# Kernel tuning notes

Hardware: AMD Instinct MI355X
Metric: run time of the kernel (lower is better)

Reference implementation:

```python
import jax, jax.numpy as jnp
import numpy as np

DIM = 512
HIDDEN = 2048
D_M = 256
R = 64
GEN_HIDDEN = D_M * 2  # hidden_mul=2
ALPHA_MEM = 1.0


def setup_inputs() -> dict:
    key = jax.random.key(0)
    ks = jax.random.split(key, 12)
    B, T = 2, 512
    inp = {
        'x': jax.random.normal(ks[0], (B, T, DIM), jnp.float32),
        'm_tok': jax.random.normal(ks[1], (B, T, D_M), jnp.float32),
        # base SwiGLU params
        'W1': jax.random.normal(ks[2], (HIDDEN, DIM), jnp.float32) * (1.0 / np.sqrt(DIM)),
        'W2': jax.random.normal(ks[3], (HIDDEN, DIM), jnp.float32) * (1.0 / np.sqrt(DIM)),
        'W3': jax.random.normal(ks[4], (DIM, HIDDEN), jnp.float32) * (1.0 / np.sqrt(HIDDEN)),
        'b1': jnp.zeros((HIDDEN,), jnp.float32),
        'b2': jnp.zeros((HIDDEN,), jnp.float32),
        'b3': jnp.zeros((DIM,), jnp.float32),
        # hypernetwork (FFNMemGenerator): d_m -> gen_hidden -> 3*r*dim
        'gen_w1': jax.random.normal(ks[5], (GEN_HIDDEN, D_M), jnp.float32) * (1.0 / np.sqrt(D_M)),
        'gen_b1': jnp.zeros((GEN_HIDDEN,), jnp.float32),
        'gen_w2': jax.random.normal(ks[6], (3 * R * DIM, GEN_HIDDEN), jnp.float32) * (0.02 / np.sqrt(GEN_HIDDEN)),
        'gen_b2': jnp.zeros((3 * R * DIM,), jnp.float32),
        'mem_gate': jnp.zeros((), jnp.float32),
    }
    return inp


def reference(x, m_tok, W1, W2, W3, b1, b2, b3, gen_w1, gen_b1, gen_w2, gen_b2, mem_gate):
    B, T, _ = x.shape
    # base SwiGLU FFN
    x1 = jnp.einsum('od,btd->bto', W1, x) + b1  # [B,T,hidden]
    x2 = jnp.einsum('od,btd->bto', W2, x) + b2
    h_base = jax.nn.silu(x1) * x2
    y_base = jnp.einsum('do,bto->btd', W3, h_base) + b3  # [B,T,dim]

    # hypernetwork-generated per-token low-rank weights
    hg = jax.nn.silu(jnp.einsum('hd,btd->bth', gen_w1, m_tok) + gen_b1)
    w = jnp.einsum('oh,bth->bto', gen_w2, hg) + gen_b2  # [B,T,3*r*dim]
    W1_m = w[..., : R * DIM].reshape(B, T, R, DIM)
    W2_m = w[..., R * DIM : 2 * R * DIM].reshape(B, T, R, DIM)
    W3_m = w[..., 2 * R * DIM :].reshape(B, T, DIM, R)

    # per-token batched matvecs (memory path)
    u1 = jnp.einsum('btrd,btd->btr', W1_m, x)
    u2 = jnp.einsum('btrd,btd->btr', W2_m, x)
    h_mem = jax.nn.silu(u1) * u2
    y_mem = jnp.einsum('btdr,btr->btd', W3_m, h_mem)

    g = jax.nn.sigmoid(mem_gate)
    return y_base + g * ALPHA_MEM * y_mem
```

## Files before the change

### kernel.cpp

```cpp
#include <hip/hip_runtime.h>
#include <cstdint>
#include <cstddef>

#define TOK   1024
#define DIMX  512
#define HID   2048
#define DM    256
#define GENH  512
#define RR    64
#define O3BASE 65536

typedef __bf16 bf16x8 __attribute__((ext_vector_type(8)));
typedef float  f32x4  __attribute__((ext_vector_type(4)));

__device__ __forceinline__ unsigned short f2bf(float f) {
  union { float f; uint32_t u; } v; v.f = f;
  return (unsigned short)((v.u + 0x7fffu + ((v.u >> 16) & 1u)) >> 16);
}
__device__ __forceinline__ float bf2f(unsigned short h) {
  union { uint32_t u; float f; } v; v.u = (uint32_t)h << 16;
  return v.f;
}
__device__ __forceinline__ float silu_f(float x) { return x / (1.f + __expf(-x)); }

__device__ __forceinline__ void async_copy16(const void* g, void* l) {
  __builtin_amdgcn_global_load_lds(
      (const __attribute__((address_space(1))) void*)g,
      (__attribute__((address_space(3))) void*)l, 16, 0, 0);
}

__device__ __forceinline__ void cast8(const float* __restrict__ src,
                                      unsigned short* __restrict__ dst, size_t i) {
  float4 v0 = *(const float4*)(src + i);
  float4 v1 = *(const float4*)(src + i + 4);
  ushort4 h0, h1;
  h0.x = f2bf(v0.x); h0.y = f2bf(v0.y); h0.z = f2bf(v0.z); h0.w = f2bf(v0.w);
  h1.x = f2bf(v1.x); h1.y = f2bf(v1.y); h1.z = f2bf(v1.z); h1.w = f2bf(v1.w);
  *(ushort4*)(dst + i)     = h0;
  *(ushort4*)(dst + i + 4) = h1;
}

__global__ __launch_bounds__(256) void cast_bf16_kernel(
    const float* __restrict__ src, unsigned short* __restrict__ dst) {
  cast8(src, dst, ((size_t)blockIdx.x * 256 + threadIdx.x) * 8);
}

template<int ROWS>
__device__ __forceinline__ void stage_tile(
    const unsigned short* __restrict__ base, size_t row0, int stride, int kofs,
    unsigned short* Ls, int tid) {
  constexpr int IT = ROWS / 32;
  const int wave = tid >> 6, lane = tid & 63;
#pragma unroll
  for (int j = 0; j < IT; ++j) {
    int s   = wave * (IT * 64) + j * 64 + lane;
    int row = s >> 3;
    int kc  = (s & 7) ^ (row & 7);
    const unsigned short* g = base + (row0 + (size_t)row) * (size_t)stride + kofs + kc * 8;
    async_copy16(g, (char*)Ls + wave * (IT * 1024) + j * 1024);
  }
}

template<int KLEN, int MF>
__device__ __forceinline__ void mfma_tile_nt(
    const unsigned short* __restrict__ Abf, size_t a_row0, int astride,
    const unsigned short* __restrict__ Bbf, size_t b_row0, int bstride, int k0,
    unsigned short* As, unsigned short* Bs, f32x4 (&acc)[MF][4]) {
  const int tid  = threadIdx.x;
  const int lane = tid & 63;
  const int wave = tid >> 6;
  const int m0 = (wave >> 1) * (MF * 16), n0 = (wave & 1) * 64;

  for (int kk = 0; kk < KLEN; kk += 64) {
    stage_tile<MF * 32>(Abf, a_row0, astride, k0 + kk, As, tid);
    stage_tile<128>(Bbf, b_row0, bstride, k0 + kk, Bs, tid);
    __syncthreads();
#pragma unroll
    for (int ks = 0; ks < 2; ++ks) {
      int cbase = ks * 4 + (lane >> 4);
      int koff  = (cbase ^ (lane & 7)) * 8;
      bf16x8 a[MF], b[4];
#pragma unroll
      for (int mf = 0; mf < MF; ++mf)
        a[mf] = *(const bf16x8*)(As + (m0 + mf * 16 + (lane & 15)) * 64 + koff);
#pragma unroll
      for (int nf = 0; nf < 4; ++nf)
        b[nf] = *(const bf16x8*)(Bs + (n0 + nf * 16 + (lane & 15)) * 64 + koff);
#pragma unroll
      for (int mf = 0; mf < MF; ++mf)
#pragma unroll
        for (int nf = 0; nf < 4; ++nf)
          acc[mf][nf] = __builtin_amdgcn_mfma_f32_16x16x32_bf16(
              a[mf], b[nf], acc[mf][nf], 0, 0, 0);
    }
    __syncthreads();
  }
}

template<int MF>
__device__ __forceinline__ void zero_accN(f32x4 (&acc)[MF][4]) {
#pragma unroll
  for (int i = 0; i < MF; ++i)
#pragma unroll
    for (int j = 0; j < 4; ++j) {
      f32x4 z = {0.f, 0.f, 0.f, 0.f};
      acc[i][j] = z;
    }
}

__global__ __launch_bounds__(256) void prep_kernel(
    const float* __restrict__ x, const float* __restrict__ m_tok,
    const float* __restrict__ gen_w1, const float* __restrict__ gen_b1,
    const float* __restrict__ W1, const float* __restrict__ W2,
    const float* __restrict__ W3,
    unsigned short* __restrict__ xb, unsigned short* __restrict__ hgb,
    unsigned short* __restrict__ W1b, unsigned short* __restrict__ W2b,
    unsigned short* __restrict__ W3b) {
  __shared__ float mt[4 * DM];
  const int tid = threadIdx.x;
  const size_t t0 = (size_t)blockIdx.x * 4;
#pragma unroll
  for (int k = 0; k < 4; ++k) mt[k * 256 + tid] = m_tok[t0 * DM + k * 256 + tid];
#pragma unroll
  for (int k = 0; k < 8; ++k) {
    size_t idx = t0 * DIMX + k * 256 + tid;
    xb[idx] = f2bf(x[idx]);
  }
  {
    size_t base = ((size_t)blockIdx.x * 256 + tid) * 8;
#pragma unroll
    for (int it = 0; it < 2; ++it) {
      size_t idx = base + (size_t)it * 524288;
      cast8(W1, W1b, idx);
      cast8(W2, W2b, idx);
      cast8(W3, W3b, idx);
    }
  }
  __syncthreads();
#pragma unroll
  for (int hh = 0; hh < 2; ++hh) {
    int h = hh * 256 + tid;
    float a0, a1, a2, a3;
    a0 = a1 = a2 = a3 = gen_b1[h];
    const float* wr = gen_w1 + (size_t)h * DM;
    for (int d = 0; d < DM; d += 4) {
      float4 w = *(const float4*)(wr + d);
      a0 += w.x * mt[d]       + w.y * mt[d + 1]       + w.z * mt[d + 2]       + w.w * mt[d + 3];
      a1 += w.x * mt[256 + d] + w.y * mt[256 + d + 1] + w.z * mt[256 + d + 2] + w.w * mt[256 + d + 3];
      a2 += w.x * mt[512 + d] + w.y * mt[512 + d + 1] + w.z * mt[512 + d + 2] + w.w * mt[512 + d + 3];
      a3 += w.x * mt[768 + d] + w.y * mt[768 + d + 1] + w.z * mt[768 + d + 2] + w.w * mt[768 + d + 3];
    }
    hgb[(t0 + 0) * GENH + h] = f2bf(silu_f(a0));
    hgb[(t0 + 1) * GENH + h] = f2bf(silu_f(a1));
    hgb[(t0 + 2) * GENH + h] = f2bf(silu_f(a2));
    hgb[(t0 + 3) * GENH + h] = f2bf(silu_f(a3));
  }
}

__global__ __launch_bounds__(256) void ffn12_kernel(
    const unsigned short* __restrict__ xb, const unsigned short* __restrict__ W1b,
    const unsigned short* __restrict__ W2b, const float* __restrict__ pb1,
    const float* __restrict__ pb2, unsigned short* __restrict__ hb) {
  __shared__ unsigned short As[32 * 64];
  __shared__ unsigned short B1s[128 * 64];
  __shared__ unsigned short B2s[128 * 64];
  const int tid = threadIdx.x, lane = tid & 63, wave = tid >> 6;
  const int ob = blockIdx.x & 15, tb = blockIdx.x >> 4;
  const size_t t0 = (size_t)tb * 32, o0 = (size_t)ob * 128;
  const int m0 = (wave >> 1) * 16, n0 = (wave & 1) * 64;

  f32x4 acc1[4], acc2[4];
#pragma unroll
  for (int j = 0; j < 4; ++j) {
    f32x4 z = {0.f, 0.f, 0.f, 0.f};
    acc1[j] = z; acc2[j] = z;
  }

  for (int kk = 0; kk < DIMX; kk += 64) {
    stage_tile<32>(xb, t0, DIMX, kk, As, tid);
    stage_tile<128>(W1b, o0, DIMX, kk, B1s, tid);
    stage_tile<128>(W2b, o0, DIMX, kk, B2s, tid);
    __syncthreads();
#pragma unroll
    for (int ks = 0; ks < 2; ++ks) {
      int cbase = ks * 4 + (lane >> 4);
      int koff  = (cbase ^ (lane & 7)) * 8;
      bf16x8 a, b1[4], b2[4];
      a = *(const bf16x8*)(As + (m0 + (lane & 15)) * 64 + koff);
#pragma unroll
      for (int nf = 0; nf < 4; ++nf) {
        b1[nf] = *(const bf16x8*)(B1s + (n0 + nf * 16 + (lane & 15)) * 64 + koff);
        b2[nf] = *(const bf16x8*)(B2s + (n0 + nf * 16 + (lane & 15)) * 64 + koff);
      }
#pragma unroll
      for (int nf = 0; nf < 4; ++nf) {
        acc1[nf] = __builtin_amdgcn_mfma_f32_16x16x32_bf16(a, b1[nf], acc1[nf], 0, 0, 0);
        acc2[nf] = __builtin_amdgcn_mfma_f32_16x16x32_bf16(a, b2[nf], acc2[nf], 0, 0, 0);
      }
    }
    __syncthreads();
  }

  const int q = lane >> 4;
  float b1v[4], b2v[4];
#pragma unroll
  for (int nf = 0; nf < 4; ++nf) {
    b1v[nf] = pb1[o0 + n0 + nf * 16 + (lane & 15)];
    b2v[nf] = pb2[o0 + n0 + nf * 16 + (lane & 15)];
  }
#pragma unroll
  for (int nf = 0; nf < 4; ++nf)
#pragma unroll
    for (int rg = 0; rg < 4; ++rg) {
      size_t trow = t0 + m0 + q * 4 + rg;
      size_t col  = o0 + n0 + nf * 16 + (lane & 15);
      float v1 = acc1[nf][rg] + b1v[nf];
      float v2 = acc2[nf][rg] + b2v[nf];
      hb[trow * HID + col] = f2bf(silu_f(v1) * v2);
    }
}

__global__ __launch_bounds__(256) void gemm3p_kernel(
    const unsigned short* __restrict__ hb, const unsigned short* __restrict__ W3b,
    float* __restrict__ yp) {
  __shared__ unsigned short As[64 * 64];
  __shared__ unsigned short Bs[128 * 64];
  const int ob = blockIdx.x & 3, tb = blockIdx.x >> 2;
  const size_t o0 = (size_t)ob * 128, t0 = (size_t)tb * 64;
  const int k0 = blockIdx.y * 512;
  f32x4 acc[2][4];
  zero_accN<2>(acc);
  mfma_tile_nt<512, 2>(hb, t0, HID, W3b, o0, HID, k0, As, Bs, acc);

  const int tid = threadIdx.x, lane = tid & 63, wave = tid >> 6;
  const int m0 = (wave >> 1) * 32, n0 = (wave & 1) * 64;
  float* out = yp + (size_t)blockIdx.y * (TOK * DIMX);
#pragma unroll
  for (int nf = 0; nf < 4; ++nf) {
    int n = n0 + nf * 16 + (lane & 15);
#pragma unroll
    for (int mf = 0; mf < 2; ++mf) {
      int mb = m0 + mf * 16 + ((lane >> 4) << 2);
#pragma unroll
      for (int rg = 0; rg < 4; ++rg)
        out[(t0 + mb + rg) * DIMX + o0 + n] = acc[mf][nf][rg];
    }
  }
}

__global__ __launch_bounds__(256) void yreduce_kernel(
    const float* __restrict__ yp, const float* __restrict__ b3,
    float* __restrict__ ybase) {
  size_t i = ((size_t)blockIdx.x * 256 + threadIdx.x) * 4;
  int d = (int)(i & (DIMX - 1));
  float4 s = *(const float4*)(b3 + d);
#pragma unroll
  for (int p = 0; p < 4; ++p) {
    float4 v = *(const float4*)(yp + (size_t)p * (TOK * DIMX) + i);
    s.x += v.x; s.y += v.y; s.z += v.z; s.w += v.w;
  }
  *(float4*)(ybase + i) = s;
}

union SmemUV {
  struct { unsigned short As[8192], Bs[8192]; } ab;
  struct { unsigned short Xs[128 * 128]; } ep;
};

__global__ __launch_bounds__(256) void memuv_kernel(
    const unsigned short* __restrict__ hgb, const unsigned short* __restrict__ w2b,
    const float* __restrict__ gen_b2, const unsigned short* __restrict__ xb,
    float* __restrict__ up) {
  __shared__ SmemUV sm;
  const int bx = blockIdx.x;
  const int s8 = bx & 7, w = bx >> 3;
  const int tb = w & 7, strip = (w >> 3) * 8 + s8;
  const size_t o0 = (size_t)strip * 128, t0 = (size_t)tb * 128;
  const int j  = strip >> 2;
  const int d0 = (strip & 3) * 128;

  f32x4 acc[4][4];
  zero_accN<4>(acc);
  mfma_tile_nt<GENH, 4>(hgb, t0, GENH, w2b, o0, GENH, 0, sm.ab.As, sm.ab.Bs, acc);

  const int tid = threadIdx.x, lane = tid & 63, wave = tid >> 6;
#pragma unroll
  for (int i = 0; i < 8; ++i) {
    int qq = i * 256 + tid;
    int row = qq >> 4, c = qq & 15;
    const unsigned short* src = xb + (t0 + (size_t)row) * DIMX + d0 + c * 8;
    ushort4 v0 = *(const ushort4*)src;
    ushort4 v1 = *(const ushort4*)(src + 4);
    int cs = c ^ (((row >> 2) & 3) << 1);
    unsigned short* dst = sm.ep.Xs + row * 128 + cs * 8;
    *(ushort4*)dst = v0;
    *(ushort4*)(dst + 4) = v1;
  }
  __syncthreads();

  const int m0 = (wave >> 1) * 64, n0 = (wave & 1) * 64;
  const int q = lane >> 4, l15 = lane & 15;
  float gbv[4];
#pragma unroll
  for (int i = 0; i < 4; ++i)
    gbv[i] = gen_b2[o0 + n0 + i * 16 + l15];

  const int p = (strip & 3) * 2 + (wave & 1);
  float* upd = up + (size_t)p * (128 * 1024) + (size_t)j * 1024 + t0;
#pragma unroll
  for (int mf = 0; mf < 4; ++mf) {
    f32x4 vals;
#pragma unroll
    for (int rg = 0; rg < 4; ++rg) {
      int trow = m0 + mf * 16 + q * 4 + rg;
      int swz  = ((trow >> 2) & 3) << 1;
      float val = 0.f;
#pragma unroll
      for (int nf = 0; nf < 4; ++nf) {
        int col = n0 + nf * 16 + l15;
        int idx = trow * 128 + (((col >> 3) ^ swz) << 3) + (col & 7);
        val += (acc[mf][nf][rg] + gbv[nf]) * bf2f(sm.ep.Xs[idx]);
      }
      val += __shfl_xor(val, 1);
      val += __shfl_xor(val, 2);
      val += __shfl_xor(val, 4);
      val += __shfl_xor(val, 8);
      vals[rg] = val;
    }
    if (l15 == 0)
      *(f32x4*)(upd + m0 + mf * 16 + q * 4) = vals;
  }
}

__global__ __launch_bounds__(256) void hmem_kernel(
    const float* __restrict__ up, float* __restrict__ hm) {
  int i = blockIdx.x * 256 + threadIdx.x;
  int t = i & 1023, r = i >> 10;
  float u1 = 0.f, u2 = 0.f;
#pragma unroll
  for (int p = 0; p < 8; ++p) {
    u1 += up[(size_t)p * (128 * 1024) + (size_t)r * 1024 + t];
    u2 += up[(size_t)p * (128 * 1024) + (size_t)(64 + r) * 1024 + t];
  }
  hm[(size_t)t * RR + r] = silu_f(u1) * u2;
}

union SmemY {
  struct { unsigned short As[8192], Bs[8192]; } ab;
  struct { float Hs[128 * 64]; } ep;
};

__global__ __launch_bounds__(256) void memy_kernel(
    const unsigned short* __restrict__ hgb, const unsigned short* __restrict__ w2b,
    const float* __restrict__ gen_b2, const float* __restrict__ hmem,
    const float* __restrict__ ybase, const float* __restrict__ mem_gate,
    float* __restrict__ y) {
  __shared__ SmemY sm;
  const int bx = blockIdx.x;
  const int s8 = bx & 7, w = bx >> 3;
  const int tb = w & 7, strip = (w >> 3) * 8 + s8;
  const size_t brow0 = (size_t)O3BASE + (size_t)strip * 128;
  const size_t t0 = (size_t)tb * 128;

  f32x4 acc[4][4];
  zero_accN<4>(acc);
  mfma_tile_nt<GENH, 4>(hgb, t0, GENH, w2b, brow0, GENH, 0, sm.ab.As, sm.ab.Bs, acc);

  const int tid = threadIdx.x, lane = tid & 63, wave = tid >> 6;
#pragma unroll
  for (int i = 0; i < 8; ++i) {
    int qq = i * 256 + tid;
    int row = qq >> 4, c = qq & 15;
    float4 v = *(const float4*)(hmem + (t0 + (size_t)row) * RR + c * 4);
    int cs = c ^ (((row >> 2) & 3) << 2);
    *(float4*)(sm.ep.Hs + row * 64 + cs * 4) = v;
  }
  __syncthreads();

  const int m0 = (wave >> 1) * 64, n0 = (wave & 1) * 64;
  const int q = lane >> 4, l15 = lane & 15;
  const float g = 1.f / (1.f + __expf(-mem_gate[0]));
  float gbv[4];
#pragma unroll
  for (int i = 0; i < 4; ++i)
    gbv[i] = gen_b2[brow0 + n0 + i * 16 + l15];

  const int d = strip * 2 + (wave & 1);
#pragma unroll
  for (int mf = 0; mf < 4; ++mf)
#pragma unroll
    for (int rg = 0; rg < 4; ++rg) {
      int trow = m0 + mf * 16 + q * 4 + rg;
      int swz  = ((trow >> 2) & 3) << 2;
      float val = 0.f;
#pragma unroll
      for (int nf = 0; nf < 4; ++nf) {
        int r = nf * 16 + l15;
        int idx = trow * 64 + (((r >> 2) ^ swz) << 2) + (r & 3);
        val += (acc[mf][nf][rg] + gbv[nf]) * sm.ep.Hs[idx];
      }
      val += __shfl_xor(val, 1);
      val += __shfl_xor(val, 2);
      val += __shfl_xor(val, 4);
      val += __shfl_xor(val, 8);
      if (l15 == 0) {
        size_t gi = (t0 + trow) * DIMX + d;
        y[gi] = ybase[gi] + g * val;
      }
    }
}

extern "C" void kernel_launch(void* const* d_in, const int* in_sizes, int n_in,
                              void* d_out, int out_size, void* d_ws, size_t ws_size,
                              hipStream_t stream) {
  const float* x        = (const float*)d_in[0];
  const float* m_tok    = (const float*)d_in[1];
  const float* W1       = (const float*)d_in[2];
  const float* W2       = (const float*)d_in[3];
  const float* W3       = (const float*)d_in[4];
  const float* b1       = (const float*)d_in[5];
  const float* b2       = (const float*)d_in[6];
  const float* b3       = (const float*)d_in[7];
  const float* gen_w1   = (const float*)d_in[8];
  const float* gen_b1   = (const float*)d_in[9];
  const float* gen_w2   = (const float*)d_in[10];
  const float* gen_b2   = (const float*)d_in[11];
  const float* mem_gate = (const float*)d_in[12];
  float* y = (float*)d_out;

  char* ws = (char*)d_ws;
#define KB(v) ((size_t)(v) << 10)
  unsigned short* xb    = (unsigned short*)(ws);
  unsigned short* hgb   = (unsigned short*)(ws + KB(1024));
  unsigned short* hb    = (unsigned short*)(ws + KB(2048));
  float* up    = (float*)(ws + KB(6144));
  float* hm    = (float*)(ws + KB(10240));
  float* yp    = (float*)(ws + KB(10752));
  float* ybase = (float*)(ws + KB(19200));
  unsigned short* W1b = (unsigned short*)(ws + KB(21248));
  unsigned short* W2b = (unsigned short*)(ws + KB(23296));
  unsigned short* W3b = (unsigned short*)(ws + KB(25344));
  unsigned short* w2b = (unsigned short*)(ws + KB(27392));
#undef KB

  prep_kernel<<<256, 256, 0, stream>>>(x, m_tok, gen_w1, gen_b1, W1, W2, W3,
                                       xb, hgb, W1b, W2b, W3b);
  cast_bf16_kernel<<<24576, 256, 0, stream>>>(gen_w2, w2b);

  ffn12_kernel<<<512, 256, 0, stream>>>(xb, W1b, W2b, b1, b2, hb);
  gemm3p_kernel<<<dim3(64, 4), 256, 0, stream>>>(hb, W3b, yp);
  yreduce_kernel<<<512, 256, 0, stream>>>(yp, b3, ybase);

  memuv_kernel<<<4096, 256, 0, stream>>>(hgb, w2b, gen_b2, xb, up);
  hmem_kernel<<<256, 256, 0, stream>>>(up, hm);
  memy_kernel<<<2048, 256, 0, stream>>>(hgb, w2b, gen_b2, hm, ybase, mem_gate, y);
}
```

Before: 528.0 us.

## Fuse gen_w2 cast into GEMM staging and merge independent kernels

Removes the separate pass that casts gen_w2 from fp32 to bf16 and instead loads fp32 gen_w2 tiles inside the memuv/memy GEMMs, converting them to bf16 in registers before writing to LDS. The ffn12 and memuv kernels are merged into one launch, as are gemm3p and hmem, with branching on block index. The yreduce kernel is folded into memy's epilogue. This saves a large 24 MB write/read round trip and several launches, but the gen_w2 tile loads become synchronous and twice as wide, since gen_w2 is read in fp32 instead of bf16 with no async copy to LDS.

New measurement: 539.7 us. 2.2% more time.

```diff
diff --git a/kernel.cpp b/kernel.cpp
--- a/kernel.cpp
+++ b/kernel.cpp
@@ -22,6 +22,13 @@
   return v.f;
 }
 __device__ __forceinline__ float silu_f(float x) { return x / (1.f + __expf(-x)); }
+
+__device__ __forceinline__ ushort4 cvt4_hw(float4 v) {
+  union { __bf16 b; unsigned short u; } r0, r1, r2, r3;
+  r0.b = (__bf16)v.x; r1.b = (__bf16)v.y; r2.b = (__bf16)v.z; r3.b = (__bf16)v.w;
+  ushort4 h; h.x = r0.u; h.y = r1.u; h.z = r2.u; h.w = r3.u;
+  return h;
+}
 
 __device__ __forceinline__ void async_copy16(const void* g, void* l) {
   __builtin_amdgcn_global_load_lds(
@@ -40,11 +47,6 @@
   *(ushort4*)(dst + i + 4) = h1;
 }
 
-__global__ __launch_bounds__(256) void cast_bf16_kernel(
-    const float* __restrict__ src, unsigned short* __restrict__ dst) {
-  cast8(src, dst, ((size_t)blockIdx.x * 256 + threadIdx.x) * 8);
-}
-
 template<int ROWS>
 __device__ __forceinline__ void stage_tile(
     const unsigned short* __restrict__ base, size_t row0, int stride, int kofs,
@@ -74,6 +76,61 @@
   for (int kk = 0; kk < KLEN; kk += 64) {
     stage_tile<MF * 32>(Abf, a_row0, astride, k0 + kk, As, tid);
     stage_tile<128>(Bbf, b_row0, bstride, k0 + kk, Bs, tid);
+    __syncthreads();
+#pragma unroll
+    for (int ks = 0; ks < 2; ++ks) {
+      int cbase = ks * 4 + (lane >> 4);
+      int koff  = (cbase ^ (lane & 7)) * 8;
+      bf16x8 a[MF], b[4];
+#pragma unroll
+      for (int mf = 0; mf < MF; ++mf)
+        a[mf] = *(const bf16x8*)(As + (m0 + mf * 16 + (lane & 15)) * 64 + koff);
+#pragma unroll
+      for (int nf = 0; nf < 4; ++nf)
+        b[nf] = *(const bf16x8*)(Bs + (n0 + nf * 16 + (lane & 15)) * 64 + koff);
+#pragma unroll
+      for (int mf = 0; mf < MF; ++mf)
+#pragma unroll
+        for (int nf = 0; nf < 4; ++nf)
+          acc[mf][nf] = __builtin_amdgcn_mfma_f32_16x16x32_bf16(
+              a[mf], b[nf], acc[mf][nf], 0, 0, 0);
+    }
+    __syncthreads();
+  }
+}
+
+template<int KLEN, int MF>
+__device__ __forceinline__ void mfma_tile_nt_bf32(
+    const unsigned short* __restrict__ Abf, size_t a_row0, int astride,
+    const float* __restrict__ Bf, size_t b_row0, int bstride, int k0,
+    unsigned short* As, unsigned short* Bs, f32x4 (&acc)[MF][4]) {
+  const int tid  = threadIdx.x;
+  const int lane = tid & 63;
+  const int wave = tid >> 6;
+  const int m0 = (wave >> 1) * (MF * 16), n0 = (wave & 1) * 64;
+
+  for (int kk = 0; kk < KLEN; kk += 64) {
+    stage_tile<MF * 32>(Abf, a_row0, astride, k0 + kk, As, tid);
+#pragma unroll
+    for (int grp = 0; grp < 2; ++grp) {
+      float4 v[4];
+#pragma unroll
+      for (int jj = 0; jj < 2; ++jj) {
+        int s   = wave * 256 + (grp * 2 + jj) * 64 + lane;
+        int row = s >> 3;
+        int kc  = (s & 7) ^ (row & 7);
+        const float* g = Bf + (b_row0 + (size_t)row) * (size_t)bstride
+                            + (k0 + kk) + kc * 8;
+        v[2 * jj]     = *(const float4*)g;
+        v[2 * jj + 1] = *(const float4*)(g + 4);
+      }
+#pragma unroll
+      for (int jj = 0; jj < 2; ++jj) {
+        int s = wave * 256 + (grp * 2 + jj) * 64 + lane;
+        *(ushort4*)(Bs + s * 8)     = cvt4_hw(v[2 * jj]);
+        *(ushort4*)(Bs + s * 8 + 4) = cvt4_hw(v[2 * jj + 1]);
+      }
+    }
     __syncthreads();
 #pragma unroll
     for (int ks = 0; ks < 2; ++ks) {
@@ -157,15 +214,13 @@
   }
 }
 
-__global__ __launch_bounds__(256) void ffn12_kernel(
-    const unsigned short* __restrict__ xb, const unsigned short* __restrict__ W1b,
+__device__ __forceinline__ void ffn12_body(
+    int bx, const unsigned short* __restrict__ xb, const unsigned short* __restrict__ W1b,
     const unsigned short* __restrict__ W2b, const float* __restrict__ pb1,
-    const float* __restrict__ pb2, unsigned short* __restrict__ hb) {
-  __shared__ unsigned short As[32 * 64];
-  __shared__ unsigned short B1s[128 * 64];
-  __shared__ unsigned short B2s[128 * 64];
+    const float* __restrict__ pb2, unsigned short* __restrict__ hb,
+    unsigned short* As, unsigned short* B1s, unsigned short* B2s) {
   const int tid = threadIdx.x, lane = tid & 63, wave = tid >> 6;
-  const int ob = blockIdx.x & 15, tb = blockIdx.x >> 4;
+  const int ob = bx & 15, tb = bx >> 4;
   const size_t t0 = (size_t)tb * 32, o0 = (size_t)ob * 128;
   const int m0 = (wave >> 1) * 16, n0 = (wave & 1) * 64;
 
@@ -220,59 +275,15 @@
     }
 }
 
-__global__ __launch_bounds__(256) void gemm3p_kernel(
-    const unsigned short* __restrict__ hb, const unsigned short* __restrict__ W3b,
-    float* __restrict__ yp) {
-  __shared__ unsigned short As[64 * 64];
-  __shared__ unsigned short Bs[128 * 64];
-  const int ob = blockIdx.x & 3, tb = blockIdx.x >> 2;
-  const size_t o0 = (size_t)ob * 128, t0 = (size_t)tb * 64;
-  const int k0 = blockIdx.y * 512;
-  f32x4 acc[2][4];
-  zero_accN<2>(acc);
-  mfma_tile_nt<512, 2>(hb, t0, HID, W3b, o0, HID, k0, As, Bs, acc);
-
-  const int tid = threadIdx.x, lane = tid & 63, wave = tid >> 6;
-  const int m0 = (wave >> 1) * 32, n0 = (wave & 1) * 64;
-  float* out = yp + (size_t)blockIdx.y * (TOK * DIMX);
-#pragma unroll
-  for (int nf = 0; nf < 4; ++nf) {
-    int n = n0 + nf * 16 + (lane & 15);
-#pragma unroll
-    for (int mf = 0; mf < 2; ++mf) {
-      int mb = m0 + mf * 16 + ((lane >> 4) << 2);
-#pragma unroll
-      for (int rg = 0; rg < 4; ++rg)
-        out[(t0 + mb + rg) * DIMX + o0 + n] = acc[mf][nf][rg];
-    }
-  }
-}
-
-__global__ __launch_bounds__(256) void yreduce_kernel(
-    const float* __restrict__ yp, const float* __restrict__ b3,
-    float* __restrict__ ybase) {
-  size_t i = ((size_t)blockIdx.x * 256 + threadIdx.x) * 4;
-  int d = (int)(i & (DIMX - 1));
-  float4 s = *(const float4*)(b3 + d);
-#pragma unroll
-  for (int p = 0; p < 4; ++p) {
-    float4 v = *(const float4*)(yp + (size_t)p * (TOK * DIMX) + i);
-    s.x += v.x; s.y += v.y; s.z += v.z; s.w += v.w;
-  }
-  *(float4*)(ybase + i) = s;
-}
-
 union SmemUV {
   struct { unsigned short As[8192], Bs[8192]; } ab;
   struct { unsigned short Xs[128 * 128]; } ep;
 };
 
-__global__ __launch_bounds__(256) void memuv_kernel(
-    const unsigned short* __restrict__ hgb, const unsigned short* __restrict__ w2b,
+__device__ __forceinline__ void memuv_body(
+    int bx, const unsigned short* __restrict__ hgb, const float* __restrict__ gw2,
     const float* __restrict__ gen_b2, const unsigned short* __restrict__ xb,
-    float* __restrict__ up) {
-  __shared__ SmemUV sm;
-  const int bx = blockIdx.x;
+    float* __restrict__ up, SmemUV& sm) {
   const int s8 = bx & 7, w = bx >> 3;
   const int tb = w & 7, strip = (w >> 3) * 8 + s8;
   const size_t o0 = (size_t)strip * 128, t0 = (size_t)tb * 128;
@@ -281,7 +292,7 @@
 
   f32x4 acc[4][4];
   zero_accN<4>(acc);
-  mfma_tile_nt<GENH, 4>(hgb, t0, GENH, w2b, o0, GENH, 0, sm.ab.As, sm.ab.Bs, acc);
+  mfma_tile_nt_bf32<GENH, 4>(hgb, t0, GENH, gw2, o0, GENH, 0, sm.ab.As, sm.ab.Bs, acc);
 
   const int tid = threadIdx.x, lane = tid & 63, wave = tid >> 6;
 #pragma unroll
@@ -332,9 +343,55 @@
   }
 }
 
-__global__ __launch_bounds__(256) void hmem_kernel(
-    const float* __restrict__ up, float* __restrict__ hm) {
-  int i = blockIdx.x * 256 + threadIdx.x;
+union SmemK2 {
+  struct { unsigned short As[32 * 64], B1s[128 * 64], B2s[128 * 64]; } f;
+  SmemUV m;
+};
+
+__global__ __launch_bounds__(256) void k2_kernel(
+    const unsigned short* __restrict__ xb, const unsigned short* __restrict__ W1b,
+    const unsigned short* __restrict__ W2b, const float* __restrict__ b1,
+    const float* __restrict__ b2, unsigned short* __restrict__ hb,
+    const unsigned short* __restrict__ hgb, const float* __restrict__ gw2,
+    const float* __restrict__ gen_b2, float* __restrict__ up) {
+  __shared__ SmemK2 sm;
+  const int bx = blockIdx.x;
+  if (bx < 512)
+    ffn12_body(bx, xb, W1b, W2b, b1, b2, hb, sm.f.As, sm.f.B1s, sm.f.B2s);
+  else
+    memuv_body(bx - 512, hgb, gw2, gen_b2, xb, up, sm.m);
+}
+
+__device__ __forceinline__ void gemm3p_body(
+    int bx, const unsigned short* __restrict__ hb, const unsigned short* __restrict__ W3b,
+    float* __restrict__ yp, unsigned short* As, unsigned short* Bs) {
+  const int slice = bx >> 6, r6 = bx & 63;
+  const int ob = r6 & 3, tb = r6 >> 2;
+  const size_t o0 = (size_t)ob * 128, t0 = (size_t)tb * 64;
+  const int k0 = slice * 512;
+  f32x4 acc[2][4];
+  zero_accN<2>(acc);
+  mfma_tile_nt<512, 2>(hb, t0, HID, W3b, o0, HID, k0, As, Bs, acc);
+
+  const int tid = threadIdx.x, lane = tid & 63, wave = tid >> 6;
+  const int m0 = (wave >> 1) * 32, n0 = (wave & 1) * 64;
+  float* out = yp + (size_t)slice * (TOK * DIMX);
+#pragma unroll
+  for (int nf = 0; nf < 4; ++nf) {
+    int n = n0 + nf * 16 + (lane & 15);
+#pragma unroll
+    for (int mf = 0; mf < 2; ++mf) {
+      int mb = m0 + mf * 16 + ((lane >> 4) << 2);
+#pragma unroll
+      for (int rg = 0; rg < 4; ++rg)
+        out[(t0 + mb + rg) * DIMX + o0 + n] = acc[mf][nf][rg];
+    }
+  }
+}
+
+__device__ __forceinline__ void hmem_body(int bx, const float* __restrict__ up,
+                                          float* __restrict__ hm) {
+  int i = bx * 256 + threadIdx.x;
   int t = i & 1023, r = i >> 10;
   float u1 = 0.f, u2 = 0.f;
 #pragma unroll
@@ -343,6 +400,21 @@
     u2 += up[(size_t)p * (128 * 1024) + (size_t)(64 + r) * 1024 + t];
   }
   hm[(size_t)t * RR + r] = silu_f(u1) * u2;
+}
+
+union SmemK3 {
+  struct { unsigned short As[64 * 64], Bs[128 * 64]; } g;
+};
+
+__global__ __launch_bounds__(256) void k3_kernel(
+    const unsigned short* __restrict__ hb, const unsigned short* __restrict__ W3b,
+    float* __restrict__ yp, const float* __restrict__ up, float* __restrict__ hm) {
+  __shared__ SmemK3 sm;
+  const int bx = blockIdx.x;
+  if (bx < 256)
+    gemm3p_body(bx, hb, W3b, yp, sm.g.As, sm.g.Bs);
+  else
+    hmem_body(bx - 256, up, hm);
 }
 
 union SmemY {
@@ -351,10 +423,10 @@
 };
 
 __global__ __launch_bounds__(256) void memy_kernel(
-    const unsigned short* __restrict__ hgb, const unsigned short* __restrict__ w2b,
+    const unsigned short* __restrict__ hgb, const float* __restrict__ gw2,
     const float* __restrict__ gen_b2, const float* __restrict__ hmem,
-    const float* __restrict__ ybase, const float* __restrict__ mem_gate,
-    float* __restrict__ y) {
+    const float* __restrict__ yp, const float* __restrict__ b3,
+    const float* __restrict__ mem_gate, float* __restrict__ y) {
   __shared__ SmemY sm;
   const int bx = blockIdx.x;
   const int s8 = bx & 7, w = bx >> 3;
@@ -364,7 +436,7 @@
 
   f32x4 acc[4][4];
   zero_accN<4>(acc);
-  mfma_tile_nt<GENH, 4>(hgb, t0, GENH, w2b, brow0, GENH, 0, sm.ab.As, sm.ab.Bs, acc);
+  mfma_tile_nt_bf32<GENH, 4>(hgb, t0, GENH, gw2, brow0, GENH, 0, sm.ab.As, sm.ab.Bs, acc);
 
   const int tid = threadIdx.x, lane = tid & 63, wave = tid >> 6;
 #pragma unroll
@@ -386,6 +458,7 @@
     gbv[i] = gen_b2[brow0 + n0 + i * 16 + l15];
 
   const int d = strip * 2 + (wave & 1);
+  const float b3v = b3[d];
 #pragma unroll
   for (int mf = 0; mf < 4; ++mf)
 #pragma unroll
@@ -405,7 +478,11 @@
       val += __shfl_xor(val, 8);
       if (l15 == 0) {
         size_t gi = (t0 + trow) * DIMX + d;
-        y[gi] = ybase[gi] + g * val;
+        float base = b3v + yp[gi]
+                   + yp[(size_t)1 * (TOK * DIMX) + gi]
+                   + yp[(size_t)2 * (TOK * DIMX) + gi]
+                   + yp[(size_t)3 * (TOK * DIMX) + gi];
+        y[gi] = base + g * val;
       }
     }
 }
@@ -430,28 +507,22 @@
 
   char* ws = (char*)d_ws;
 #define KB(v) ((size_t)(v) << 10)
-  unsigned short* xb    = (unsigned short*)(ws);
-  unsigned short* hgb   = (unsigned short*)(ws + KB(1024));
-  unsigned short* hb    = (unsigned short*)(ws + KB(2048));
-  float* up    = (float*)(ws + KB(6144));
-  float* hm    = (float*)(ws + KB(10240));
-  float* yp    = (float*)(ws + KB(10752));
-  float* ybase = (float*)(ws + KB(19200));
+  unsigned short* xb  = (unsigned short*)(ws);
+  unsigned short* hgb = (unsigned short*)(ws + KB(1024));
+  unsigned short* hb  = (unsigned short*)(ws + KB(2048));
+  float* up  = (float*)(ws + KB(6144));
+  float* hm  = (float*)(ws + KB(10240));
+  float* yp  = (float*)(ws + KB(10752));
   unsigned short* W1b = (unsigned short*)(ws + KB(21248));
   unsigned short* W2b = (unsigned short*)(ws + KB(23296));
   unsigned short* W3b = (unsigned short*)(ws + KB(25344));
-  unsigned short* w2b = (unsigned short*)(ws + KB(27392));
 #undef KB
 
   prep_kernel<<<256, 256, 0, stream>>>(x, m_tok, gen_w1, gen_b1, W1, W2, W3,
                                        xb, hgb, W1b, W2b, W3b);
-  cast_bf16_kernel<<<24576, 256, 0, stream>>>(gen_w2, w2b);
-
-  ffn12_kernel<<<512, 256, 0, stream>>>(xb, W1b, W2b, b1, b2, hb);
-  gemm3p_kernel<<<dim3(64, 4), 256, 0, stream>>>(hb, W3b, yp);
-  yreduce_kernel<<<512, 256, 0, stream>>>(yp, b3, ybase);
-
-  memuv_kernel<<<4096, 256, 0, stream>>>(hgb, w2b, gen_b2, xb, up);
-  hmem_kernel<<<256, 256, 0, stream>>>(up, hm);
-  memy_kernel<<<2048, 256, 0, stream>>>(hgb, w2b, gen_b2, hm, ybase, mem_gate, y);
-}
+  k2_kernel<<<512 + 4096, 256, 0, stream>>>(xb, W1b, W2b, b1, b2, hb,
+                                            hgb, gen_w2, gen_b2, up);
+  k3_kernel<<<256 + 256, 256, 0, stream>>>(hb, W3b, yp, up, hm);
+  memy_kernel<<<2048, 256, 0, stream>>>(hgb, gen_w2, gen_b2, hm, yp, b3,
+                                        mem_gate, y);
+}
```
